# Optimization experiments

Measured on AMD Instinct MI355X. Metric: run time of the kernel, lower is better.

The kernel has to match this reference:

```python
import jax, jax.numpy as jnp
import numpy as np

N = 100000
F_IN = 128
HID = 8
HEADS = 8
CLASSES = 40
NEG_SLOPE = 0.2


def gat_conv(x, src, dst, W, a_src, a_dst, bias, heads, out_c):
    # x: [N, F]; W: [F, heads*out_c]; a_src/a_dst: [heads, out_c]; bias: [heads*out_c]
    n = x.shape[0]
    h = (x @ W).reshape(n, heads, out_c)                       # [N, H, C]
    al_src = jnp.sum(h * a_src, axis=-1)                       # [N, H]
    al_dst = jnp.sum(h * a_dst, axis=-1)                       # [N, H]
    e = jax.nn.leaky_relu(al_src[src] + al_dst[dst], NEG_SLOPE)  # [E, H]
    # segment softmax over destination node (PyG softmax over edge_index[1])
    m = jax.ops.segment_max(e, dst, num_segments=n)            # [N, H]
    m = jnp.where(jnp.isfinite(m), m, 0.0)
    ex = jnp.exp(e - m[dst])
    denom = jax.ops.segment_sum(ex, dst, num_segments=n)       # [N, H]
    alpha = ex / denom[dst]                                    # [E, H]
    msg = h[src] * alpha[:, :, None]                           # [E, H, C]
    out = jax.ops.segment_sum(msg, dst, num_segments=n)        # [N, H, C]
    return out.reshape(n, heads * out_c) + bias


def setup_inputs() -> dict:
    key = jax.random.key(0)
    ks = jax.random.split(key, 12)
    E = 1600000
    x = jax.random.normal(ks[0], (N, F_IN), dtype=jnp.float32)
    edge_index = jax.random.randint(ks[1], (2, E), 0, N, dtype=jnp.int32)
    # layer 1: in=F_IN, out=HID, heads=HEADS, concat -> 64 channels
    s1 = 1.0 / np.sqrt(F_IN)
    W1 = jax.random.uniform(ks[2], (F_IN, HEADS * HID), jnp.float32, -s1, s1)
    a_src1 = jax.random.uniform(ks[3], (HEADS, HID), jnp.float32, -0.3, 0.3)
    a_dst1 = jax.random.uniform(ks[4], (HEADS, HID), jnp.float32, -0.3, 0.3)
    b1 = jnp.zeros((HEADS * HID,), jnp.float32)
    # layer 2: in=64, out=CLASSES, heads=1
    d2 = HEADS * HID
    s2 = 1.0 / np.sqrt(d2)
    W2 = jax.random.uniform(ks[5], (d2, CLASSES), jnp.float32, -s2, s2)
    a_src2 = jax.random.uniform(ks[6], (1, CLASSES), jnp.float32, -0.3, 0.3)
    a_dst2 = jax.random.uniform(ks[7], (1, CLASSES), jnp.float32, -0.3, 0.3)
    b2 = jnp.zeros((CLASSES,), jnp.float32)
    return {"x": x, "edge_index": edge_index, "W1": W1, "a_src1": a_src1,
            "a_dst1": a_dst1, "b1": b1, "W2": W2, "a_src2": a_src2,
            "a_dst2": a_dst2, "b2": b2}


def reference(x, edge_index, W1, a_src1, a_dst1, b1, W2, a_src2, a_dst2, b2):
    # PyG GATConv adds self-loops by default
    loops = jnp.arange(N, dtype=edge_index.dtype)
    src = jnp.concatenate([edge_index[0], loops])
    dst = jnp.concatenate([edge_index[1], loops])
    h = gat_conv(x, src, dst, W1, a_src1, a_dst1, b1, HEADS, HID)
    h = jax.nn.relu(h)  # dropout is identity in eval mode
    out = gat_conv(h, src, dst, W2, a_src2, a_dst2, b2, 1, CLASSES)
    return jax.nn.log_softmax(out, axis=1)
```

## Files before the change

### kernel.cpp

```cpp
#include <hip/hip_runtime.h>
#include <hip/hip_bf16.h>
#include <math.h>

#define FIN 128
#define HID 8
#define HEADS 8
#define C1 64
#define CLS 40
#define NSLOPE 0.2f
#define NINF (-__builtin_inff())

typedef __hip_bfloat16 bf16;

__device__ __forceinline__ float lrelu(float x) { return x >= 0.f ? x : NSLOPE * x; }

__global__ void k_deg(const int* __restrict__ ei, int E, int* __restrict__ deg) {
    int idx = blockIdx.x * blockDim.x + threadIdx.x;
    int e0 = idx * 4;
    if (e0 + 3 < E) {
        int4 dv = ((const int4*)(ei + E))[idx];
        atomicAdd(&deg[dv.x], 1); atomicAdd(&deg[dv.y], 1);
        atomicAdd(&deg[dv.z], 1); atomicAdd(&deg[dv.w], 1);
    } else {
        int e_end = min(e0 + 4, E);
        for (int e = e0; e < e_end; ++e) atomicAdd(&deg[ei[E + e]], 1);
    }
}

__global__ __launch_bounds__(256) void k_scan1(const int* __restrict__ deg,
    int* __restrict__ rowstart, int* __restrict__ bsum, int n) {
    __shared__ int sm[256];
    int t = threadIdx.x, i = blockIdx.x * 256 + t;
    int v = (i < n) ? deg[i] + 1 : 0;
    sm[t] = v; __syncthreads();
    int x = v;
    for (int off = 1; off < 256; off <<= 1) {
        int tv = (t >= off) ? sm[t - off] : 0;
        __syncthreads();
        x += tv; sm[t] = x; __syncthreads();
    }
    if (i < n) rowstart[i] = x - v;
    if (t == 255) bsum[blockIdx.x] = x;
}

__global__ __launch_bounds__(512) void k_scan2(int* __restrict__ bsum, int nb) {
    __shared__ int sm[512];
    int t = threadIdx.x;
    int v = (t < nb) ? bsum[t] : 0;
    sm[t] = v; __syncthreads();
    int x = v;
    for (int off = 1; off < 512; off <<= 1) {
        int tv = (t >= off) ? sm[t - off] : 0;
        __syncthreads();
        x += tv; sm[t] = x; __syncthreads();
    }
    if (t < nb) bsum[t] = x - v;
}

__global__ void k_scan3(int* __restrict__ rowstart, const int* __restrict__ bsum,
                        int n, int total) {
    int i = blockIdx.x * blockDim.x + threadIdx.x;
    if (i < n) rowstart[i] += bsum[i >> 8];
    if (i == 0) rowstart[n] = total;
}

__global__ __launch_bounds__(256) void k_scatter(const int* __restrict__ ei,
    int E, int En, int n, int* __restrict__ rowcur, int* __restrict__ csr) {
    int g = blockIdx.x & 7;
    int per8 = (n + 7) >> 3;
    int lo = g * per8, hi = min(n, lo + per8);
    int idx = (blockIdx.x >> 3) * 256 + threadIdx.x;
    int e0 = idx * 4;
    if (e0 + 3 < E) {
        int4 dv = ((const int4*)(ei + E))[idx];
        int4 sv = ((const int4*)ei)[idx];
        if (dv.x >= lo && dv.x < hi) csr[atomicAdd(&rowcur[dv.x], 1)] = sv.x;
        if (dv.y >= lo && dv.y < hi) csr[atomicAdd(&rowcur[dv.y], 1)] = sv.y;
        if (dv.z >= lo && dv.z < hi) csr[atomicAdd(&rowcur[dv.z], 1)] = sv.z;
        if (dv.w >= lo && dv.w < hi) csr[atomicAdd(&rowcur[dv.w], 1)] = sv.w;
    } else {
        int e_end = min(e0 + 4, En);
        for (int e = e0; e < e_end; ++e) {
            int s, d;
            if (e < E) { s = ei[e]; d = ei[E + e]; } else { s = d = e - E; }
            if (d >= lo && d < hi) csr[atomicAdd(&rowcur[d], 1)] = s;
        }
    }
}

__global__ __launch_bounds__(256) void gemm1_kernel(
    const float* __restrict__ x, const float* __restrict__ W1,
    const float* __restrict__ a_src, const float* __restrict__ a_dst,
    bf16* __restrict__ h1b, float* __restrict__ alS, float* __restrict__ alD, int n) {
    __shared__ float4 Wl[FIN][C1 / 4];
    __shared__ float xs[64][FIN + 4];
    int t = threadIdx.x;
    const float4* W4 = (const float4*)W1;
    for (int i = t; i < FIN * (C1 / 4); i += 256) Wl[i / (C1 / 4)][i % (C1 / 4)] = W4[i];
    int node0 = blockIdx.x * 64;
    for (int i = t; i < 64 * (FIN / 4); i += 256) {
        int r = i / (FIN / 4), c = i % (FIN / 4);
        int nn = node0 + r;
        float4 v = {0.f, 0.f, 0.f, 0.f};
        if (nn < n) v = ((const float4*)x)[(size_t)nn * (FIN / 4) + c];
        *(float4*)&xs[r][c * 4] = v;
    }
    __syncthreads();
    int cg = t & 15, ng = t >> 4;
    int head = cg >> 1, hc = (cg & 1) * 4;
    float acc[4][4];
    #pragma unroll
    for (int i = 0; i < 4; ++i)
        for (int j = 0; j < 4; ++j) acc[i][j] = 0.f;
    #pragma unroll 2
    for (int k = 0; k < FIN; ++k) {
        float4 w = Wl[k][cg];
        #pragma unroll
        for (int i = 0; i < 4; ++i) {
            float xv = xs[ng * 4 + i][k];
            acc[i][0] += xv * w.x; acc[i][1] += xv * w.y;
            acc[i][2] += xv * w.z; acc[i][3] += xv * w.w;
        }
    }
    float a_s[4], a_d[4];
    #pragma unroll
    for (int j = 0; j < 4; ++j) {
        a_s[j] = a_src[head * HID + hc + j];
        a_d[j] = a_dst[head * HID + hc + j];
    }
    #pragma unroll
    for (int i = 0; i < 4; ++i) {
        int node = node0 + ng * 4 + i;
        float as = acc[i][0] * a_s[0] + acc[i][1] * a_s[1]
                 + acc[i][2] * a_s[2] + acc[i][3] * a_s[3];
        float ad = acc[i][0] * a_d[0] + acc[i][1] * a_d[1]
                 + acc[i][2] * a_d[2] + acc[i][3] * a_d[3];
        as += __shfl_xor(as, 1, 64);
        ad += __shfl_xor(ad, 1, 64);
        if (node < n) {
            union { ushort4 u; bf16 b[4]; } pk;
            #pragma unroll
            for (int j = 0; j < 4; ++j) pk.b[j] = __float2bfloat16(acc[i][j]);
            ((ushort4*)h1b)[(size_t)node * (C1 / 4) + cg] = pk.u;
            if ((cg & 1) == 0) {
                alS[node * HEADS + head] = as;
                alD[node * HEADS + head] = ad;
            }
        }
    }
}

__global__ __launch_bounds__(256) void gemm2_kernel(
    const float* __restrict__ x2, const float* __restrict__ W2,
    const float* __restrict__ a_src, const float* __restrict__ a_dst,
    bf16* __restrict__ h2b, float* __restrict__ alS, float* __restrict__ alD, int n) {
    __shared__ float Wl[C1][CLS];
    __shared__ float xs[64][C1 + 4];
    int t = threadIdx.x;
    for (int i = t; i < C1 * CLS; i += 256) Wl[i / CLS][i % CLS] = W2[i];
    int node0 = blockIdx.x * 64;
    for (int i = t; i < 64 * (C1 / 4); i += 256) {
        int r = i / (C1 / 4), c = i % (C1 / 4);
        int nn = node0 + r;
        float4 v = {0.f, 0.f, 0.f, 0.f};
        if (nn < n) v = ((const float4*)x2)[(size_t)nn * (C1 / 4) + c];
        *(float4*)&xs[r][c * 4] = v;
    }
    __syncthreads();
    int cg = t & 15, ng = t >> 4;
    bool act = cg < (CLS / 4);
    float acc[4][4];
    #pragma unroll
    for (int i = 0; i < 4; ++i)
        for (int j = 0; j < 4; ++j) acc[i][j] = 0.f;
    if (act) {
        #pragma unroll 2
        for (int k = 0; k < C1; ++k) {
            float4 w = ((const float4*)&Wl[k][0])[cg];
            #pragma unroll
            for (int i = 0; i < 4; ++i) {
                float xv = xs[ng * 4 + i][k];
                acc[i][0] += xv * w.x; acc[i][1] += xv * w.y;
                acc[i][2] += xv * w.z; acc[i][3] += xv * w.w;
            }
        }
    }
    float a_s[4] = {0.f, 0.f, 0.f, 0.f}, a_d[4] = {0.f, 0.f, 0.f, 0.f};
    if (act) {
        #pragma unroll
        for (int j = 0; j < 4; ++j) {
            a_s[j] = a_src[cg * 4 + j];
            a_d[j] = a_dst[cg * 4 + j];
        }
    }
    #pragma unroll
    for (int i = 0; i < 4; ++i) {
        int node = node0 + ng * 4 + i;
        float as = acc[i][0] * a_s[0] + acc[i][1] * a_s[1]
                 + acc[i][2] * a_s[2] + acc[i][3] * a_s[3];
        float ad = acc[i][0] * a_d[0] + acc[i][1] * a_d[1]
                 + acc[i][2] * a_d[2] + acc[i][3] * a_d[3];
        #pragma unroll
        for (int off = 1; off < 16; off <<= 1) {
            as += __shfl_xor(as, off, 64);
            ad += __shfl_xor(ad, off, 64);
        }
        if (node < n) {
            if (act) {
                union { ushort4 u; bf16 b[4]; } pk;
                #pragma unroll
                for (int j = 0; j < 4; ++j) pk.b[j] = __float2bfloat16(acc[i][j]);
                ((ushort4*)h2b)[(size_t)node * (CLS / 4) + cg] = pk.u;
            }
            if (cg == 0) { alS[node] = as; alD[node] = ad; }
        }
    }
}

__global__ __launch_bounds__(256) void k_agg1(
    const int* __restrict__ csr, const int* __restrict__ rowend,
    const int* __restrict__ deg,
    const float* __restrict__ alS, const float* __restrict__ alD,
    const bf16* __restrict__ h1b, const float* __restrict__ b1,
    float* __restrict__ x2, int n) {
    __shared__ int    ls[4][64];
    __shared__ float4 lp4[4][128];
    int lane = threadIdx.x & 63, wv = threadIdx.x >> 6;
    int d = blockIdx.x * 4 + wv;
    if (d >= n) return;
    float4 ad0 = *(const float4*)(alD + d * HEADS);
    float4 ad1 = *(const float4*)(alD + d * HEADS + 4);
    float adh[8] = {ad0.x, ad0.y, ad0.z, ad0.w, ad1.x, ad1.y, ad1.z, ad1.w};
    int cnt  = deg[d] + 1;
    int base = rowend[d] - cnt;
    int hsel = lane >> 3;
    float acc = 0.f, den = 0.f;
    const float* lpf = (const float*)&lp4[wv][0];
    for (int jb = 0; jb < cnt; jb += 64) {
        int ec = min(64, cnt - jb);
        int jj = jb + lane;
        bool on = jj < cnt;
        int s = on ? csr[base + jj] : 0;
        ls[wv][lane] = s;
        float4 a0 = *(const float4*)(alS + s * HEADS);
        float4 a1 = *(const float4*)(alS + s * HEADS + 4);
        float av[8] = {a0.x, a0.y, a0.z, a0.w, a1.x, a1.y, a1.z, a1.w};
        float pv[8];
        #pragma unroll
        for (int h = 0; h < 8; ++h)
            pv[h] = on ? __expf(lrelu(av[h] + adh[h])) : 0.f;
        lp4[wv][lane * 2]     = make_float4(pv[0], pv[1], pv[2], pv[3]);
        lp4[wv][lane * 2 + 1] = make_float4(pv[4], pv[5], pv[6], pv[7]);
        int j = 0;
        for (; j + 4 <= ec; j += 4) {
            int s0 = ls[wv][j],     s1 = ls[wv][j + 1];
            int s2 = ls[wv][j + 2], s3 = ls[wv][j + 3];
            float p0 = lpf[(j    ) * 8 + hsel], p1 = lpf[(j + 1) * 8 + hsel];
            float p2 = lpf[(j + 2) * 8 + hsel], p3 = lpf[(j + 3) * 8 + hsel];
            float v0 = __bfloat162float(h1b[s0 * C1 + lane]);
            float v1 = __bfloat162float(h1b[s1 * C1 + lane]);
            float v2 = __bfloat162float(h1b[s2 * C1 + lane]);
            float v3 = __bfloat162float(h1b[s3 * C1 + lane]);
            acc = fmaf(p0, v0, acc); acc = fmaf(p1, v1, acc);
            acc = fmaf(p2, v2, acc); acc = fmaf(p3, v3, acc);
            den += p0 + p1 + p2 + p3;
        }
        for (; j < ec; ++j) {
            int s0 = ls[wv][j];
            float p0 = lpf[j * 8 + hsel];
            acc = fmaf(p0, __bfloat162float(h1b[s0 * C1 + lane]), acc);
            den += p0;
        }
    }
    float v = acc / den + b1[lane];
    x2[d * C1 + lane] = v > 0.f ? v : 0.f;
}

__global__ __launch_bounds__(256) void k_agg2(
    const int* __restrict__ csr, const int* __restrict__ rowend,
    const int* __restrict__ deg,
    const float* __restrict__ alS, const float* __restrict__ alD,
    const bf16* __restrict__ h2b, const float* __restrict__ b2,
    float* __restrict__ out, int n) {
    __shared__ int2 lsp[4][64];
    int lane = threadIdx.x & 63, wv = threadIdx.x >> 6;
    int d = blockIdx.x * 4 + wv;
    if (d >= n) return;
    float ad = alD[d];
    int cnt  = deg[d] + 1;
    int base = rowend[d] - cnt;
    bool act = lane < CLS;
    float acc = 0.f, den = 0.f;
    for (int jb = 0; jb < cnt; jb += 64) {
        int ec = min(64, cnt - jb);
        int jj = jb + lane;
        bool on = jj < cnt;
        int s = on ? csr[base + jj] : 0;
        float p = on ? __expf(lrelu(alS[s] + ad)) : 0.f;
        den += p;
        lsp[wv][lane] = make_int2(s, __float_as_int(p));
        if (act) {
            int j = 0;
            for (; j + 4 <= ec; j += 4) {
                int2 e0 = lsp[wv][j],     e1 = lsp[wv][j + 1];
                int2 e2 = lsp[wv][j + 2], e3 = lsp[wv][j + 3];
                float v0 = __bfloat162float(h2b[e0.x * CLS + lane]);
                float v1 = __bfloat162float(h2b[e1.x * CLS + lane]);
                float v2 = __bfloat162float(h2b[e2.x * CLS + lane]);
                float v3 = __bfloat162float(h2b[e3.x * CLS + lane]);
                acc = fmaf(__int_as_float(e0.y), v0, acc);
                acc = fmaf(__int_as_float(e1.y), v1, acc);
                acc = fmaf(__int_as_float(e2.y), v2, acc);
                acc = fmaf(__int_as_float(e3.y), v3, acc);
            }
            for (; j < ec; ++j) {
                int2 e0 = lsp[wv][j];
                acc = fmaf(__int_as_float(e0.y),
                           __bfloat162float(h2b[e0.x * CLS + lane]), acc);
            }
        }
    }
    #pragma unroll
    for (int off = 1; off < 64; off <<= 1) den += __shfl_xor(den, off, 64);
    float v = act ? (acc / den + b2[lane]) : NINF;
    float mx = v;
    #pragma unroll
    for (int off = 1; off < 64; off <<= 1) mx = fmaxf(mx, __shfl_xor(mx, off, 64));
    float ev = act ? __expf(v - mx) : 0.f;
    float sum = ev;
    #pragma unroll
    for (int off = 1; off < 64; off <<= 1) sum += __shfl_xor(sum, off, 64);
    float lse = mx + __logf(sum);
    if (act) out[d * CLS + lane] = v - lse;
}

extern "C" void kernel_launch(void* const* d_in, const int* in_sizes, int n_in,
                              void* d_out, int out_size, void* d_ws, size_t ws_size,
                              hipStream_t stream) {
    const float* x   = (const float*)d_in[0];
    const int*   ei  = (const int*)d_in[1];
    const float* W1  = (const float*)d_in[2];
    const float* aS1 = (const float*)d_in[3];
    const float* aD1 = (const float*)d_in[4];
    const float* b1  = (const float*)d_in[5];
    const float* W2  = (const float*)d_in[6];
    const float* aS2 = (const float*)d_in[7];
    const float* aD2 = (const float*)d_in[8];
    const float* b2  = (const float*)d_in[9];
    float* out = (float*)d_out;

    int n = in_sizes[0] / FIN;
    int E = in_sizes[1] / 2;
    int En = E + n;

    char* wsb = (char*)d_ws;
    bf16*  h1b = (bf16*)wsb;
    float* x2  = (float*)(wsb + (size_t)n * C1 * 2);
    float* alS = x2 + (size_t)n * C1;
    float* alD = alS + (size_t)n * HEADS;
    int*   csr = (int*)(alD + (size_t)n * HEADS);
    int*   rowstart = csr + En;
    int*   deg = rowstart + n + 1;
    int*   bsum = deg + n;

    const int T = 256;
    int nb = (n + 255) / 256;

    hipMemsetAsync(deg, 0, (size_t)n * sizeof(int), stream);
    k_deg<<<(E / 4 + T - 1) / T, T, 0, stream>>>(ei, E, deg);
    k_scan1<<<nb, T, 0, stream>>>(deg, rowstart, bsum, n);
    k_scan2<<<1, 512, 0, stream>>>(bsum, nb);
    k_scan3<<<nb, T, 0, stream>>>(rowstart, bsum, n, En);
    int chunks = (En + 1023) / 1024;
    k_scatter<<<chunks * 8, T, 0, stream>>>(ei, E, En, n, rowstart, csr);

    gemm1_kernel<<<(n + 63) / 64, T, 0, stream>>>(x, W1, aS1, aD1, h1b, alS, alD, n);
    k_agg1<<<(n + 3) / 4, T, 0, stream>>>(csr, rowstart, deg, alS, alD, h1b, b1, x2, n);

    gemm2_kernel<<<(n + 63) / 64, T, 0, stream>>>(x2, W2, aS2, aD2, h1b, alS, alD, n);
    k_agg2<<<(n + 3) / 4, T, 0, stream>>>(csr, rowstart, deg, alS, alD, h1b, b2, out, n);
}
```

Baseline: 355.1 us.

## Fuse layer-2 GEMM into layer-1 aggregation; partition degree atomics by node range

The layer-2 linear transform and attention-logit computation are folded into the epilogue of the layer-1 aggregation kernel. Each wavefront stores its ReLU'd 64-wide row in shared memory and multiplies it by W2, which is staged in LDS per block. This removes the x2 round-trip through global memory and one kernel launch, at the cost of reloading W2 into LDS for every 4-node block. The degree-count kernel is also split into 8 node-range groups to localise atomics, and the edge-index loads in it and in the scatter kernel use nontemporal loads.

```diff
diff --git a/kernel.cpp b/kernel.cpp
--- a/kernel.cpp
+++ b/kernel.cpp
@@ -11,19 +11,32 @@
 #define NINF (-__builtin_inff())
 
 typedef __hip_bfloat16 bf16;
+typedef int vint4 __attribute__((ext_vector_type(4)));
 
 __device__ __forceinline__ float lrelu(float x) { return x >= 0.f ? x : NSLOPE * x; }
-
-__global__ void k_deg(const int* __restrict__ ei, int E, int* __restrict__ deg) {
-    int idx = blockIdx.x * blockDim.x + threadIdx.x;
+__device__ __forceinline__ vint4 ldnt4(const int* p) {
+    return __builtin_nontemporal_load((const vint4*)p);
+}
+
+__global__ __launch_bounds__(256) void k_deg(const int* __restrict__ ei, int E,
+                                             int n, int* __restrict__ deg) {
+    int g = blockIdx.x & 7;
+    int per8 = (n + 7) >> 3;
+    int lo = g * per8, hi = min(n, lo + per8);
+    int idx = (blockIdx.x >> 3) * 256 + threadIdx.x;
     int e0 = idx * 4;
     if (e0 + 3 < E) {
-        int4 dv = ((const int4*)(ei + E))[idx];
-        atomicAdd(&deg[dv.x], 1); atomicAdd(&deg[dv.y], 1);
-        atomicAdd(&deg[dv.z], 1); atomicAdd(&deg[dv.w], 1);
+        vint4 dv = ldnt4(ei + E + e0);
+        if (dv.x >= lo && dv.x < hi) atomicAdd(&deg[dv.x], 1);
+        if (dv.y >= lo && dv.y < hi) atomicAdd(&deg[dv.y], 1);
+        if (dv.z >= lo && dv.z < hi) atomicAdd(&deg[dv.z], 1);
+        if (dv.w >= lo && dv.w < hi) atomicAdd(&deg[dv.w], 1);
     } else {
         int e_end = min(e0 + 4, E);
-        for (int e = e0; e < e_end; ++e) atomicAdd(&deg[ei[E + e]], 1);
+        for (int e = e0; e < e_end; ++e) {
+            int dd = ei[E + e];
+            if (dd >= lo && dd < hi) atomicAdd(&deg[dd], 1);
+        }
     }
 }
 
@@ -72,8 +85,8 @@
     int idx = (blockIdx.x >> 3) * 256 + threadIdx.x;
     int e0 = idx * 4;
     if (e0 + 3 < E) {
-        int4 dv = ((const int4*)(ei + E))[idx];
-        int4 sv = ((const int4*)ei)[idx];
+        vint4 dv = ldnt4(ei + E + e0);
+        vint4 sv = ldnt4(ei + e0);
         if (dv.x >= lo && dv.x < hi) csr[atomicAdd(&rowcur[dv.x], 1)] = sv.x;
         if (dv.y >= lo && dv.y < hi) csr[atomicAdd(&rowcur[dv.y], 1)] = sv.y;
         if (dv.z >= lo && dv.z < hi) csr[atomicAdd(&rowcur[dv.z], 1)] = sv.z;
@@ -150,82 +163,23 @@
     }
 }
 
-__global__ __launch_bounds__(256) void gemm2_kernel(
-    const float* __restrict__ x2, const float* __restrict__ W2,
-    const float* __restrict__ a_src, const float* __restrict__ a_dst,
-    bf16* __restrict__ h2b, float* __restrict__ alS, float* __restrict__ alD, int n) {
-    __shared__ float Wl[C1][CLS];
-    __shared__ float xs[64][C1 + 4];
-    int t = threadIdx.x;
-    for (int i = t; i < C1 * CLS; i += 256) Wl[i / CLS][i % CLS] = W2[i];
-    int node0 = blockIdx.x * 64;
-    for (int i = t; i < 64 * (C1 / 4); i += 256) {
-        int r = i / (C1 / 4), c = i % (C1 / 4);
-        int nn = node0 + r;
-        float4 v = {0.f, 0.f, 0.f, 0.f};
-        if (nn < n) v = ((const float4*)x2)[(size_t)nn * (C1 / 4) + c];
-        *(float4*)&xs[r][c * 4] = v;
-    }
-    __syncthreads();
-    int cg = t & 15, ng = t >> 4;
-    bool act = cg < (CLS / 4);
-    float acc[4][4];
-    #pragma unroll
-    for (int i = 0; i < 4; ++i)
-        for (int j = 0; j < 4; ++j) acc[i][j] = 0.f;
-    if (act) {
-        #pragma unroll 2
-        for (int k = 0; k < C1; ++k) {
-            float4 w = ((const float4*)&Wl[k][0])[cg];
-            #pragma unroll
-            for (int i = 0; i < 4; ++i) {
-                float xv = xs[ng * 4 + i][k];
-                acc[i][0] += xv * w.x; acc[i][1] += xv * w.y;
-                acc[i][2] += xv * w.z; acc[i][3] += xv * w.w;
-            }
-        }
-    }
-    float a_s[4] = {0.f, 0.f, 0.f, 0.f}, a_d[4] = {0.f, 0.f, 0.f, 0.f};
-    if (act) {
-        #pragma unroll
-        for (int j = 0; j < 4; ++j) {
-            a_s[j] = a_src[cg * 4 + j];
-            a_d[j] = a_dst[cg * 4 + j];
-        }
-    }
-    #pragma unroll
-    for (int i = 0; i < 4; ++i) {
-        int node = node0 + ng * 4 + i;
-        float as = acc[i][0] * a_s[0] + acc[i][1] * a_s[1]
-                 + acc[i][2] * a_s[2] + acc[i][3] * a_s[3];
-        float ad = acc[i][0] * a_d[0] + acc[i][1] * a_d[1]
-                 + acc[i][2] * a_d[2] + acc[i][3] * a_d[3];
-        #pragma unroll
-        for (int off = 1; off < 16; off <<= 1) {
-            as += __shfl_xor(as, off, 64);
-            ad += __shfl_xor(ad, off, 64);
-        }
-        if (node < n) {
-            if (act) {
-                union { ushort4 u; bf16 b[4]; } pk;
-                #pragma unroll
-                for (int j = 0; j < 4; ++j) pk.b[j] = __float2bfloat16(acc[i][j]);
-                ((ushort4*)h2b)[(size_t)node * (CLS / 4) + cg] = pk.u;
-            }
-            if (cg == 0) { alS[node] = as; alD[node] = ad; }
-        }
-    }
-}
-
 __global__ __launch_bounds__(256) void k_agg1(
     const int* __restrict__ csr, const int* __restrict__ rowend,
     const int* __restrict__ deg,
     const float* __restrict__ alS, const float* __restrict__ alD,
     const bf16* __restrict__ h1b, const float* __restrict__ b1,
-    float* __restrict__ x2, int n) {
+    const float* __restrict__ W2, const float* __restrict__ aS2,
+    const float* __restrict__ aD2,
+    bf16* __restrict__ h2b, float* __restrict__ alS2, float* __restrict__ alD2,
+    int n) {
     __shared__ int    ls[4][64];
     __shared__ float4 lp4[4][128];
-    int lane = threadIdx.x & 63, wv = threadIdx.x >> 6;
+    __shared__ float  xrow[4][64];
+    __shared__ float  Wl[C1][CLS];
+    int t = threadIdx.x;
+    for (int i = t; i < C1 * CLS; i += 256) Wl[i / CLS][i % CLS] = W2[i];
+    __syncthreads();
+    int lane = t & 63, wv = t >> 6;
     int d = blockIdx.x * 4 + wv;
     if (d >= n) return;
     float4 ad0 = *(const float4*)(alD + d * HEADS);
@@ -273,7 +227,23 @@
         }
     }
     float v = acc / den + b1[lane];
-    x2[d * C1 + lane] = v > 0.f ? v : 0.f;
+    v = v > 0.f ? v : 0.f;
+    xrow[wv][lane] = v;
+    bool act = lane < CLS;
+    float h2c = 0.f;
+    if (act) {
+        #pragma unroll 8
+        for (int k = 0; k < C1; ++k) h2c = fmaf(xrow[wv][k], Wl[k][lane], h2c);
+    }
+    float as2 = act ? h2c * aS2[lane] : 0.f;
+    float ad2 = act ? h2c * aD2[lane] : 0.f;
+    #pragma unroll
+    for (int off = 1; off < 64; off <<= 1) {
+        as2 += __shfl_xor(as2, off, 64);
+        ad2 += __shfl_xor(ad2, off, 64);
+    }
+    if (act) h2b[d * CLS + lane] = __float2bfloat16(h2c);
+    if (lane == 0) { alS2[d] = as2; alD2[d] = ad2; }
 }
 
 __global__ __launch_bounds__(256) void k_agg2(
@@ -354,29 +324,32 @@
     int En = E + n;
 
     char* wsb = (char*)d_ws;
-    bf16*  h1b = (bf16*)wsb;
-    float* x2  = (float*)(wsb + (size_t)n * C1 * 2);
-    float* alS = x2 + (size_t)n * C1;
-    float* alD = alS + (size_t)n * HEADS;
-    int*   csr = (int*)(alD + (size_t)n * HEADS);
+    bf16*  h1b  = (bf16*)wsb;
+    bf16*  h2b  = h1b + (size_t)n * C1;
+    float* alS1 = (float*)(h2b + (size_t)n * CLS);
+    float* alD1 = alS1 + (size_t)n * HEADS;
+    float* alS2 = alD1 + (size_t)n * HEADS;
+    float* alD2 = alS2 + n;
+    int*   csr  = (int*)(alD2 + n);
     int*   rowstart = csr + En;
-    int*   deg = rowstart + n + 1;
+    int*   deg  = rowstart + n + 1;
     int*   bsum = deg + n;
 
     const int T = 256;
     int nb = (n + 255) / 256;
 
-    hipMemsetAsync(deg, 0, (size_t)n * sizeof(int), stream);
-    k_deg<<<(E / 4 + T - 1) / T, T, 0, stream>>>(ei, E, deg);
+    (void)hipMemsetAsync(deg, 0, (size_t)n * sizeof(int), stream);
+    int chunksD = (E / 4 + T - 1) / T;
+    k_deg<<<chunksD * 8, T, 0, stream>>>(ei, E, n, deg);
     k_scan1<<<nb, T, 0, stream>>>(deg, rowstart, bsum, n);
     k_scan2<<<1, 512, 0, stream>>>(bsum, nb);
     k_scan3<<<nb, T, 0, stream>>>(rowstart, bsum, n, En);
     int chunks = (En + 1023) / 1024;
     k_scatter<<<chunks * 8, T, 0, stream>>>(ei, E, En, n, rowstart, csr);
 
-    gemm1_kernel<<<(n + 63) / 64, T, 0, stream>>>(x, W1, aS1, aD1, h1b, alS, alD, n);
-    k_agg1<<<(n + 3) / 4, T, 0, stream>>>(csr, rowstart, deg, alS, alD, h1b, b1, x2, n);
-
-    gemm2_kernel<<<(n + 63) / 64, T, 0, stream>>>(x2, W2, aS2, aD2, h1b, alS, alD, n);
-    k_agg2<<<(n + 3) / 4, T, 0, stream>>>(csr, rowstart, deg, alS, alD, h1b, b2, out, n);
-}
+    gemm1_kernel<<<(n + 63) / 64, T, 0, stream>>>(x, W1, aS1, aD1, h1b, alS1, alD1, n);
+    k_agg1<<<(n + 3) / 4, T, 0, stream>>>(csr, rowstart, deg, alS1, alD1, h1b, b1,
+                                          W2, aS2, aD2, h2b, alS2, alD2, n);
+
+    k_agg2<<<(n + 3) / 4, T, 0, stream>>>(csr, rowstart, deg, alS2, alD2, h2b, b2, out, n);
+}
```

New measurement: 389.8 us. +9.8%, slower.
